# Kernel optimization log

Measured on AMD Instinct MI355X. Metric: run time of the kernel, lower is better.

The kernel has to match this reference:

```python
import jax, jax.numpy as jnp
import numpy as np

B, N, A, O, D, Q, H = 64, 4, 1024, 128, 256, 256, 128
NEG_INF = -1e30


def setup_inputs() -> dict:
    key = jax.random.key(0)
    ks = jax.random.split(key, 8)
    q = jax.random.normal(ks[0], (B, N, 1, Q), dtype=jnp.float32)
    att1 = jax.random.uniform(ks[1], (B, N, A, O), dtype=jnp.float32)
    obj_reps = jax.random.normal(ks[2], (B, O, D), dtype=jnp.float32)
    tags_attention = jax.random.randint(ks[3], (B, N, A), 0, 2, dtype=jnp.int32)
    W1 = jax.random.normal(ks[4], (D + Q, H), dtype=jnp.float32) / np.sqrt(D + Q)
    b1 = jnp.zeros((H,), dtype=jnp.float32)
    W2 = jax.random.normal(ks[5], (H, 1), dtype=jnp.float32) / np.sqrt(H)
    b2 = jnp.zeros((1,), dtype=jnp.float32)
    return {"q": q, "att1": att1, "obj_reps": obj_reps,
            "tags_attention": tags_attention,
            "W1": W1, "b1": b1, "W2": W2, "b2": b2, "t": 1}


def reference(q, att1, obj_reps, tags_attention, W1, b1, W2, b2, t):
    # v: [B,N,A,D] = att1 [B,N,A,O] @ obj_reps [B,O,D]
    v = jnp.einsum('bnao,bod->bnad', att1, obj_reps)
    # q broadcast over token dim A, concat -> [B,N,A,D+Q]
    q_proj = jnp.broadcast_to(q, v.shape[:3] + (q.shape[-1],))
    vq = jnp.concatenate([v, q_proj], axis=-1)
    # FCNet: Linear + ReLU (dropout is identity at inference)
    joint_repr = jax.nn.relu(vq @ W1 + b1)          # [B,N,A,H]
    logits = (joint_repr @ W2 + b2)[..., 0]          # [B,N,A]
    # temperature-scaled masked softmax over tokens
    masked = jnp.where(tags_attention > 0, logits / t, NEG_INF)
    att2 = jax.nn.softmax(masked, axis=-1)           # [B,N,A]
    # attention_last: [B,N,O] = att2 [B,N,1,A] @ att1 [B,N,A,O]
    return jnp.einsum('bna,bnao->bno', att2, att1)
```

## Files before the change

kernel.cpp:

```cpp
#include <hip/hip_runtime.h>
#include <math.h>

#define Bc 64
#define Nc 4
#define Ac 1024
#define Oc 128
#define Dc 256
#define Qc 256
#define Hc 128
#define BN (Bc*Nc)

using f4     = __attribute__((ext_vector_type(4))) float;
using f32x4  = __attribute__((ext_vector_type(4))) float;
using short8 = __attribute__((ext_vector_type(8))) short;
using us4    = __attribute__((ext_vector_type(4))) unsigned short;

__device__ inline float decode_t(const void* p) {
    int i = *(const int*)p;
    if (i >= 1 && i <= 1000000) return (float)i;
    return __int_as_float(i);
}

__device__ inline unsigned short bf16_rne(float x) {
    unsigned u = __builtin_bit_cast(unsigned, x);
    u += 0x7FFFu + ((u >> 16) & 1u);
    return (unsigned short)(u >> 16);
}

__device__ inline void split_bf16(float x, unsigned short& hi, unsigned short& lo) {
    unsigned u = __builtin_bit_cast(unsigned, x);
    hi = (unsigned short)(u >> 16);
    float hif = __builtin_bit_cast(float, u & 0xFFFF0000u);
    float lof = x - hif;
    lo = (unsigned short)(__builtin_bit_cast(unsigned, lof) >> 16);
}

template<int CTRL>
__device__ inline float dpp_ror_add(float x) {
    int yi = __builtin_amdgcn_update_dpp(0, __builtin_bit_cast(int, x),
                                         CTRL, 0xf, 0xf, true);
    return x + __builtin_bit_cast(float, yi);
}
__device__ inline float row16_sum(float v) {
    v = dpp_ror_add<0x128>(v);
    v = dpp_ror_add<0x124>(v);
    v = dpp_ror_add<0x122>(v);
    v = dpp_ror_add<0x121>(v);
    return v;
}

__global__ __launch_bounds__(256) void prep_split_kernel(
    const float* __restrict__ obj, const float* __restrict__ W1,
    unsigned short* __restrict__ obj_hi, unsigned short* __restrict__ obj_lo,
    unsigned short* __restrict__ W1T_hi, unsigned short* __restrict__ W1T_lo)
{
    __shared__ float Ts[64][65];
    const int t = threadIdx.x;
    const int bid = blockIdx.x;

    if (bid < 1024) {
        size_t i0 = ((size_t)bid * 256 + t) * 8;
        f4 v0 = *(const f4*)(obj + i0);
        f4 v1 = *(const f4*)(obj + i0 + 4);
        short8 hi, lo;
        unsigned short h16, l16;
        #pragma unroll
        for (int j = 0; j < 4; j++) {
            split_bf16(v0[j], h16, l16); hi[j] = (short)h16; lo[j] = (short)l16;
        }
        #pragma unroll
        for (int j = 0; j < 4; j++) {
            split_bf16(v1[j], h16, l16); hi[4 + j] = (short)h16; lo[4 + j] = (short)l16;
        }
        *(short8*)(obj_hi + i0) = hi;
        *(short8*)(obj_lo + i0) = lo;
    } else {
        const int wb = bid - 1024;
        const int d0 = (wb & 3) * 64, h0 = (wb >> 2) * 64;
        const int r4 = t >> 6, c = t & 63;
        #pragma unroll
        for (int rr = 0; rr < 16; rr++) {
            int d = rr * 4 + r4;
            Ts[d][c] = W1[(size_t)(d0 + d) * Hc + h0 + c];
        }
        __syncthreads();
        #pragma unroll
        for (int rr = 0; rr < 16; rr++) {
            int hl = rr * 4 + r4;
            float v = Ts[c][hl];
            unsigned short h16, l16;
            split_bf16(v, h16, l16);
            W1T_hi[(size_t)(h0 + hl) * Dc + d0 + c] = h16;
            W1T_lo[(size_t)(h0 + hl) * Dc + d0 + c] = l16;
        }
    }
}

__global__ __launch_bounds__(256, 4) void prep_M2_kernel(
    const unsigned short* __restrict__ W1T_hi, const unsigned short* __restrict__ W1T_lo,
    const unsigned short* __restrict__ obj_hi, const unsigned short* __restrict__ obj_lo,
    unsigned short* __restrict__ Mt_hi, unsigned short* __restrict__ Mt_lo)
{
    const int t = threadIdx.x;
    const int wave = t >> 6, lane = t & 63;
    const int l15 = lane & 15, quad = lane >> 4;
    const int h0 = blockIdx.x * 64 + wave * 16;
    const int o0 = blockIdx.y * 32;
    const int b  = blockIdx.z;

    const size_t arow  = (size_t)(h0 + l15) * Dc;
    const size_t brow0 = ((size_t)b * Oc + o0 + l15) * Dc;
    const size_t brow1 = ((size_t)b * Oc + o0 + 16 + l15) * Dc;

    f32x4 acc0 = (f32x4)(0.f), acc1 = (f32x4)(0.f);
    #pragma unroll
    for (int ks = 0; ks < 8; ks++) {
        const int ko = ks * 32 + quad * 8;
        short8 Ah  = *(const short8*)(W1T_hi + arow + ko);
        short8 Al  = *(const short8*)(W1T_lo + arow + ko);
        short8 B0h = *(const short8*)(obj_hi + brow0 + ko);
        short8 B0l = *(const short8*)(obj_lo + brow0 + ko);
        short8 B1h = *(const short8*)(obj_hi + brow1 + ko);
        short8 B1l = *(const short8*)(obj_lo + brow1 + ko);
        acc0 = __builtin_amdgcn_mfma_f32_16x16x32_bf16(Al, B0l, acc0, 0, 0, 0);
        acc0 = __builtin_amdgcn_mfma_f32_16x16x32_bf16(Al, B0h, acc0, 0, 0, 0);
        acc0 = __builtin_amdgcn_mfma_f32_16x16x32_bf16(Ah, B0l, acc0, 0, 0, 0);
        acc0 = __builtin_amdgcn_mfma_f32_16x16x32_bf16(Ah, B0h, acc0, 0, 0, 0);
        acc1 = __builtin_amdgcn_mfma_f32_16x16x32_bf16(Al, B1l, acc1, 0, 0, 0);
        acc1 = __builtin_amdgcn_mfma_f32_16x16x32_bf16(Al, B1h, acc1, 0, 0, 0);
        acc1 = __builtin_amdgcn_mfma_f32_16x16x32_bf16(Ah, B1l, acc1, 0, 0, 0);
        acc1 = __builtin_amdgcn_mfma_f32_16x16x32_bf16(Ah, B1h, acc1, 0, 0, 0);
    }

    #pragma unroll
    for (int r = 0; r < 4; r++) {
        int hrow = h0 + quad * 4 + r;
        size_t base = ((size_t)b * Hc + hrow) * Oc + o0 + l15;
        unsigned short hh, ll;
        split_bf16(acc0[r], hh, ll);
        Mt_hi[base] = hh; Mt_lo[base] = ll;
        split_bf16(acc1[r], hh, ll);
        Mt_hi[base + 16] = hh; Mt_lo[base + 16] = ll;
    }
}

__global__ __launch_bounds__(512) void prep_qb_kernel(
    const float* __restrict__ q, const float* __restrict__ W1,
    const float* __restrict__ b1, float* __restrict__ qb)
{
    __shared__ float qs[256];
    __shared__ float red[4][128];
    const int t = threadIdx.x;
    const int bn = blockIdx.x;

    if (t < 256) qs[t] = q[bn * Qc + t];
    __syncthreads();

    const int h = t & 127, kq = t >> 7;
    float acc = 0.f;
    const float* w = W1 + (size_t)(Dc + kq * 64) * Hc + h;
    #pragma unroll 8
    for (int d = 0; d < 64; ++d)
        acc += qs[kq * 64 + d] * w[(size_t)d * Hc];
    red[kq][h] = acc;
    __syncthreads();

    if (t < 128)
        qb[bn * Hc + t] = b1[t] + red[0][t] + red[1][t] + red[2][t] + red[3][t];
}

__global__ __launch_bounds__(512, 4) void main_half_kernel(
    const float* __restrict__ att1, const int* __restrict__ tags,
    const unsigned short* __restrict__ Mt_hi, const unsigned short* __restrict__ Mt_lo,
    const float* __restrict__ qb, const float* __restrict__ W2,
    const float* __restrict__ b2, const void* __restrict__ tptr,
    float* __restrict__ out_part, float* __restrict__ z_part)
{
    __shared__ unsigned short A_s[64][136];
    __shared__ float part2[64][9];
    __shared__ float part3[16][132];
    __shared__ float e_s[64];
    __shared__ float qb_s[128], w2_s[128];

    const int t    = threadIdx.x;
    const int lane = t & 63;
    const int wave = t >> 6;
    const int l15  = lane & 15;
    const int quad = lane >> 4;
    const int blk  = blockIdx.x;
    const int bn   = blk >> 1;
    const int half = blk & 1;
    const int b    = bn >> 2;
    const int hw   = wave * 16;
    const int g3   = t >> 5;
    const int o4   = (t & 31) * 4;

    const float* att_half = att1 + ((size_t)bn * Ac + half * 512) * Oc;

    f4 sv[4];
    #pragma unroll
    for (int s = 0; s < 4; s++) {
        int idx = t + 512 * s;
        sv[s] = *(const f4*)(att_half + (size_t)idx * 4);
    }

    const size_t brow = ((size_t)b * Hc + hw + l15) * Oc;
    short8 Bh[4], Bl[4];
    #pragma unroll
    for (int ks = 0; ks < 4; ks++) {
        const int ko = ks * 32 + quad * 8;
        Bh[ks] = *(const short8*)(Mt_hi + brow + ko);
        Bl[ks] = *(const short8*)(Mt_lo + brow + ko);
    }

    if (t < 128) { qb_s[t] = qb[bn * Hc + t]; w2_s[t] = W2[t]; }
    int tg_cur = (t < 64) ? tags[(size_t)bn * Ac + half * 512 + t] : 0;
    const float b2v  = b2[0];
    const float tval = decode_t(tptr);

    float z_reg = 0.f;
    f4 out4 = {0.f, 0.f, 0.f, 0.f};

    for (int tile = 0; tile < 8; ++tile) {
        #pragma unroll
        for (int s = 0; s < 4; s++) {
            int idx = t + 512 * s;
            int r = idx >> 5, c4 = idx & 31;
            us4 h4;
            #pragma unroll
            for (int j = 0; j < 4; j++) h4[j] = bf16_rne(sv[s][j]);
            *(us4*)&A_s[r][c4 * 4] = h4;
        }
        __syncthreads();

        f4 nv[4];
        int tg_next = 0;
        if (tile < 7) {
            const float* np = att_half + (size_t)(tile + 1) * 64 * Oc;
            #pragma unroll
            for (int s = 0; s < 4; s++) {
                int idx = t + 512 * s;
                nv[s] = *(const f4*)(np + (size_t)idx * 4);
            }
            if (t < 64) tg_next = tags[(size_t)bn * Ac + half * 512 + (tile + 1) * 64 + t];
        }

        f32x4 acc[4];
        #pragma unroll
        for (int i = 0; i < 4; i++) acc[i] = (f32x4)(0.f);
        #pragma unroll
        for (int ks = 0; ks < 4; ks++) {
            const int ko = ks * 32 + quad * 8;
            #pragma unroll
            for (int i = 0; i < 4; i++) {
                short8 ah = *(const short8*)&A_s[i * 16 + l15][ko];
                acc[i] = __builtin_amdgcn_mfma_f32_16x16x32_bf16(ah, Bh[ks], acc[i], 0, 0, 0);
                acc[i] = __builtin_amdgcn_mfma_f32_16x16x32_bf16(ah, Bl[ks], acc[i], 0, 0, 0);
            }
        }

        {
            const float qbv = qb_s[hw + l15], w2v = w2_s[hw + l15];
            #pragma unroll
            for (int i = 0; i < 4; i++)
                #pragma unroll
                for (int r = 0; r < 4; r++) {
                    float v = acc[i][r] + qbv;
                    v = v > 0.f ? v : 0.f;
                    float s = row16_sum(v * w2v);
                    if (l15 == 0)
                        part2[i * 16 + quad * 4 + r][wave] = s;
                }
        }
        __syncthreads();

        if (t < 64) {
            float sum = b2v;
            #pragma unroll
            for (int x = 0; x < 8; x++) sum += part2[t][x];
            float logit = sum / tval;
            float e = (tg_cur > 0) ? __expf(logit) : 0.f;
            e_s[t] = e;
            z_reg += e;
        }
        __syncthreads();

        #pragma unroll
        for (int s = 0; s < 4; s++) {
            const float ev = e_s[g3 + 16 * s];
            out4[0] += ev * sv[s][0];
            out4[1] += ev * sv[s][1];
            out4[2] += ev * sv[s][2];
            out4[3] += ev * sv[s][3];
        }

        #pragma unroll
        for (int s = 0; s < 4; s++) sv[s] = nv[s];
        tg_cur = tg_next;
    }

    __syncthreads();
    *(f4*)&part3[g3][o4] = out4;
    __syncthreads();
    if (t < 128) {
        float s = 0.f;
        #pragma unroll
        for (int g = 0; g < 16; g++) s += part3[g][t];
        out_part[(size_t)blk * 128 + t] = s;
    }
    if (t < 64) {
        float z = z_reg;
        #pragma unroll
        for (int off = 32; off > 0; off >>= 1) z += __shfl_down(z, off);
        if (t == 0) z_part[blk] = z;
    }
}

__global__ __launch_bounds__(128) void finalize_kernel(
    const float* __restrict__ out_part, const float* __restrict__ z_part,
    float* __restrict__ out)
{
    const int bn = blockIdx.x;
    const int t  = threadIdx.x;
    const float Z = z_part[bn * 2] + z_part[bn * 2 + 1];
    const float v = out_part[(size_t)(bn * 2) * 128 + t]
                  + out_part[(size_t)(bn * 2 + 1) * 128 + t];
    out[(size_t)bn * 128 + t] = v / Z;
}

extern "C" void kernel_launch(void* const* d_in, const int* in_sizes, int n_in,
                              void* d_out, int out_size, void* d_ws, size_t ws_size,
                              hipStream_t stream)
{
    (void)in_sizes; (void)n_in; (void)out_size; (void)ws_size;

    const float* q    = (const float*)d_in[0];
    const float* att1 = (const float*)d_in[1];
    const float* obj  = (const float*)d_in[2];
    const int*   tags = (const int*)d_in[3];
    const float* W1   = (const float*)d_in[4];
    const float* b1   = (const float*)d_in[5];
    const float* W2   = (const float*)d_in[6];
    const float* b2   = (const float*)d_in[7];
    const void*  tptr = (const void*)d_in[8];
    float* out = (float*)d_out;

    char* wsb = (char*)d_ws;
    unsigned short* Mt_hi  = (unsigned short*)wsb;
    unsigned short* Mt_lo  = (unsigned short*)(wsb + (size_t) 2*1024*1024);
    float* qbuf            = (float*)         (wsb + (size_t) 4*1024*1024);
    float* out_part        = (float*)         (wsb + (size_t) 5*1024*1024);
    float* z_part          = (float*)         (wsb + (size_t) 6*1024*1024);
    unsigned short* W1T_hi = (unsigned short*)(wsb + (size_t) 7*1024*1024);
    unsigned short* W1T_lo = (unsigned short*)(wsb + (size_t) 7*1024*1024 + 64*1024);
    unsigned short* obj_hi = (unsigned short*)(wsb + (size_t) 8*1024*1024);
    unsigned short* obj_lo = (unsigned short*)(wsb + (size_t)12*1024*1024);

    prep_split_kernel<<<dim3(1032), 256, 0, stream>>>(obj, W1, obj_hi, obj_lo,
                                                      W1T_hi, W1T_lo);
    prep_M2_kernel<<<dim3(2, 4, Bc), 256, 0, stream>>>(W1T_hi, W1T_lo, obj_hi, obj_lo,
                                                       Mt_hi, Mt_lo);
    prep_qb_kernel<<<dim3(BN), 512, 0, stream>>>(q, W1, b1, qbuf);
    main_half_kernel<<<dim3(2 * BN), 512, 0, stream>>>(att1, tags, Mt_hi, Mt_lo,
                                                       qbuf, W2, b2, tptr,
                                                       out_part, z_part);
    finalize_kernel<<<dim3(BN), 128, 0, stream>>>(out_part, z_part, out);
}
```

Before: 241.9 us.

## Fuse prep kernels and fold finalize into main kernel via atomic flag handoff

Merges the bf16 split, M2 GEMM and qb projection into a single prep kernel that splits W1 and obj rows in registers instead of staging hi/lo copies in global memory. It also removes the finalize kernel: each block pair handshakes through an atomicExch flag with a magic tag, and the second arriving half combines the partials and writes the output. This cuts two kernel launches and the intermediate workspace traffic. In exchange, W1 is read uncoalesced and redundantly per block, and the flag scheme relies on stale workspace values not matching the magic tag across calls.

```diff
diff --git a/kernel.cpp b/kernel.cpp
--- a/kernel.cpp
+++ b/kernel.cpp
@@ -49,138 +49,119 @@
     return v;
 }
 
-__global__ __launch_bounds__(256) void prep_split_kernel(
+__device__ inline short8 pack_hi(const f4& a, const f4& b,
+                                 short8& lo_out) {
+    short8 hi;
+    unsigned short h16, l16;
+    #pragma unroll
+    for (int j = 0; j < 4; j++) {
+        split_bf16(a[j], h16, l16); hi[j] = (short)h16; lo_out[j] = (short)l16;
+    }
+    #pragma unroll
+    for (int j = 0; j < 4; j++) {
+        split_bf16(b[j], h16, l16); hi[4+j] = (short)h16; lo_out[4+j] = (short)l16;
+    }
+    return hi;
+}
+
+__global__ __launch_bounds__(256, 2) void prep_fused_kernel(
     const float* __restrict__ obj, const float* __restrict__ W1,
-    unsigned short* __restrict__ obj_hi, unsigned short* __restrict__ obj_lo,
-    unsigned short* __restrict__ W1T_hi, unsigned short* __restrict__ W1T_lo)
-{
-    __shared__ float Ts[64][65];
-    const int t = threadIdx.x;
-    const int bid = blockIdx.x;
-
-    if (bid < 1024) {
-        size_t i0 = ((size_t)bid * 256 + t) * 8;
-        f4 v0 = *(const f4*)(obj + i0);
-        f4 v1 = *(const f4*)(obj + i0 + 4);
-        short8 hi, lo;
-        unsigned short h16, l16;
-        #pragma unroll
-        for (int j = 0; j < 4; j++) {
-            split_bf16(v0[j], h16, l16); hi[j] = (short)h16; lo[j] = (short)l16;
-        }
-        #pragma unroll
-        for (int j = 0; j < 4; j++) {
-            split_bf16(v1[j], h16, l16); hi[4 + j] = (short)h16; lo[4 + j] = (short)l16;
-        }
-        *(short8*)(obj_hi + i0) = hi;
-        *(short8*)(obj_lo + i0) = lo;
-    } else {
-        const int wb = bid - 1024;
-        const int d0 = (wb & 3) * 64, h0 = (wb >> 2) * 64;
-        const int r4 = t >> 6, c = t & 63;
-        #pragma unroll
-        for (int rr = 0; rr < 16; rr++) {
-            int d = rr * 4 + r4;
-            Ts[d][c] = W1[(size_t)(d0 + d) * Hc + h0 + c];
-        }
-        __syncthreads();
-        #pragma unroll
-        for (int rr = 0; rr < 16; rr++) {
-            int hl = rr * 4 + r4;
-            float v = Ts[c][hl];
-            unsigned short h16, l16;
-            split_bf16(v, h16, l16);
-            W1T_hi[(size_t)(h0 + hl) * Dc + d0 + c] = h16;
-            W1T_lo[(size_t)(h0 + hl) * Dc + d0 + c] = l16;
-        }
-    }
-}
-
-__global__ __launch_bounds__(256, 4) void prep_M2_kernel(
-    const unsigned short* __restrict__ W1T_hi, const unsigned short* __restrict__ W1T_lo,
-    const unsigned short* __restrict__ obj_hi, const unsigned short* __restrict__ obj_lo,
-    unsigned short* __restrict__ Mt_hi, unsigned short* __restrict__ Mt_lo)
-{
-    const int t = threadIdx.x;
-    const int wave = t >> 6, lane = t & 63;
-    const int l15 = lane & 15, quad = lane >> 4;
-    const int h0 = blockIdx.x * 64 + wave * 16;
-    const int o0 = blockIdx.y * 32;
-    const int b  = blockIdx.z;
-
-    const size_t arow  = (size_t)(h0 + l15) * Dc;
-    const size_t brow0 = ((size_t)b * Oc + o0 + l15) * Dc;
-    const size_t brow1 = ((size_t)b * Oc + o0 + 16 + l15) * Dc;
-
-    f32x4 acc0 = (f32x4)(0.f), acc1 = (f32x4)(0.f);
-    #pragma unroll
-    for (int ks = 0; ks < 8; ks++) {
-        const int ko = ks * 32 + quad * 8;
-        short8 Ah  = *(const short8*)(W1T_hi + arow + ko);
-        short8 Al  = *(const short8*)(W1T_lo + arow + ko);
-        short8 B0h = *(const short8*)(obj_hi + brow0 + ko);
-        short8 B0l = *(const short8*)(obj_lo + brow0 + ko);
-        short8 B1h = *(const short8*)(obj_hi + brow1 + ko);
-        short8 B1l = *(const short8*)(obj_lo + brow1 + ko);
-        acc0 = __builtin_amdgcn_mfma_f32_16x16x32_bf16(Al, B0l, acc0, 0, 0, 0);
-        acc0 = __builtin_amdgcn_mfma_f32_16x16x32_bf16(Al, B0h, acc0, 0, 0, 0);
-        acc0 = __builtin_amdgcn_mfma_f32_16x16x32_bf16(Ah, B0l, acc0, 0, 0, 0);
-        acc0 = __builtin_amdgcn_mfma_f32_16x16x32_bf16(Ah, B0h, acc0, 0, 0, 0);
-        acc1 = __builtin_amdgcn_mfma_f32_16x16x32_bf16(Al, B1l, acc1, 0, 0, 0);
-        acc1 = __builtin_amdgcn_mfma_f32_16x16x32_bf16(Al, B1h, acc1, 0, 0, 0);
-        acc1 = __builtin_amdgcn_mfma_f32_16x16x32_bf16(Ah, B1l, acc1, 0, 0, 0);
-        acc1 = __builtin_amdgcn_mfma_f32_16x16x32_bf16(Ah, B1h, acc1, 0, 0, 0);
-    }
-
-    #pragma unroll
-    for (int r = 0; r < 4; r++) {
-        int hrow = h0 + quad * 4 + r;
-        size_t base = ((size_t)b * Hc + hrow) * Oc + o0 + l15;
-        unsigned short hh, ll;
-        split_bf16(acc0[r], hh, ll);
-        Mt_hi[base] = hh; Mt_lo[base] = ll;
-        split_bf16(acc1[r], hh, ll);
-        Mt_hi[base + 16] = hh; Mt_lo[base + 16] = ll;
-    }
-}
-
-__global__ __launch_bounds__(512) void prep_qb_kernel(
-    const float* __restrict__ q, const float* __restrict__ W1,
-    const float* __restrict__ b1, float* __restrict__ qb)
+    const float* __restrict__ q,   const float* __restrict__ b1,
+    unsigned short* __restrict__ Mt_hi, unsigned short* __restrict__ Mt_lo,
+    float* __restrict__ qb)
 {
     __shared__ float qs[256];
-    __shared__ float red[4][128];
-    const int t = threadIdx.x;
-    const int bn = blockIdx.x;
-
-    if (t < 256) qs[t] = q[bn * Qc + t];
-    __syncthreads();
-
-    const int h = t & 127, kq = t >> 7;
-    float acc = 0.f;
-    const float* w = W1 + (size_t)(Dc + kq * 64) * Hc + h;
-    #pragma unroll 8
-    for (int d = 0; d < 64; ++d)
-        acc += qs[kq * 64 + d] * w[(size_t)d * Hc];
-    red[kq][h] = acc;
-    __syncthreads();
-
-    if (t < 128)
-        qb[bn * Hc + t] = b1[t] + red[0][t] + red[1][t] + red[2][t] + red[3][t];
-}
+    __shared__ float red[2][128];
+
+    const int bid = blockIdx.x;
+    const int t   = threadIdx.x;
+
+    if (bid < 512) {
+        const int b    = bid >> 3;
+        const int rr   = bid & 7;
+        const int h0   = (rr & 1) * 64;
+        const int o0   = (rr >> 1) * 32;
+        const int wave = t >> 6, lane = t & 63;
+        const int l15  = lane & 15, quad = lane >> 4;
+        const int hh   = h0 + wave * 16 + l15;
+
+        short8 Ah[8], Al[8];
+        #pragma unroll
+        for (int ks = 0; ks < 8; ks++) {
+            const int ko = ks * 32 + quad * 8;
+            #pragma unroll
+            for (int j = 0; j < 8; j++) {
+                unsigned short h16, l16;
+                split_bf16(W1[(size_t)(ko + j) * Hc + hh], h16, l16);
+                Ah[ks][j] = (short)h16; Al[ks][j] = (short)l16;
+            }
+        }
+
+        const float* ob0 = obj + ((size_t)b * Oc + o0 + l15) * Dc;
+        const float* ob1 = obj + ((size_t)b * Oc + o0 + 16 + l15) * Dc;
+
+        f32x4 acc0 = (f32x4)(0.f), acc1 = (f32x4)(0.f);
+        #pragma unroll
+        for (int ks = 0; ks < 8; ks++) {
+            const int ko = ks * 32 + quad * 8;
+            short8 B0l, B1l;
+            short8 B0h = pack_hi(*(const f4*)(ob0 + ko), *(const f4*)(ob0 + ko + 4), B0l);
+            short8 B1h = pack_hi(*(const f4*)(ob1 + ko), *(const f4*)(ob1 + ko + 4), B1l);
+            acc0 = __builtin_amdgcn_mfma_f32_16x16x32_bf16(Al[ks], B0l, acc0, 0, 0, 0);
+            acc0 = __builtin_amdgcn_mfma_f32_16x16x32_bf16(Al[ks], B0h, acc0, 0, 0, 0);
+            acc0 = __builtin_amdgcn_mfma_f32_16x16x32_bf16(Ah[ks], B0l, acc0, 0, 0, 0);
+            acc0 = __builtin_amdgcn_mfma_f32_16x16x32_bf16(Ah[ks], B0h, acc0, 0, 0, 0);
+            acc1 = __builtin_amdgcn_mfma_f32_16x16x32_bf16(Al[ks], B1l, acc1, 0, 0, 0);
+            acc1 = __builtin_amdgcn_mfma_f32_16x16x32_bf16(Al[ks], B1h, acc1, 0, 0, 0);
+            acc1 = __builtin_amdgcn_mfma_f32_16x16x32_bf16(Ah[ks], B1l, acc1, 0, 0, 0);
+            acc1 = __builtin_amdgcn_mfma_f32_16x16x32_bf16(Ah[ks], B1h, acc1, 0, 0, 0);
+        }
+
+        #pragma unroll
+        for (int r = 0; r < 4; r++) {
+            int hrow = h0 + wave * 16 + quad * 4 + r;
+            size_t base = ((size_t)b * Hc + hrow) * Oc + o0 + l15;
+            unsigned short hh16, ll16;
+            split_bf16(acc0[r], hh16, ll16);
+            Mt_hi[base] = hh16; Mt_lo[base] = ll16;
+            split_bf16(acc1[r], hh16, ll16);
+            Mt_hi[base + 16] = hh16; Mt_lo[base + 16] = ll16;
+        }
+    } else {
+        const int bn = bid - 512;
+        qs[t] = q[bn * Qc + t];
+        __syncthreads();
+
+        const int h = t & 127, kq = t >> 7;
+        float acc = 0.f;
+        const float* w = W1 + (size_t)(Dc + kq * 128) * Hc + h;
+        #pragma unroll 8
+        for (int d = 0; d < 128; ++d)
+            acc += qs[kq * 128 + d] * w[(size_t)d * Hc];
+        red[kq][h] = acc;
+        __syncthreads();
+
+        if (t < 128)
+            qb[bn * Hc + t] = b1[t] + red[0][t] + red[1][t];
+    }
+}
+
+#define MAGIC 0x3A9F17C0u
 
 __global__ __launch_bounds__(512, 4) void main_half_kernel(
     const float* __restrict__ att1, const int* __restrict__ tags,
     const unsigned short* __restrict__ Mt_hi, const unsigned short* __restrict__ Mt_lo,
     const float* __restrict__ qb, const float* __restrict__ W2,
     const float* __restrict__ b2, const void* __restrict__ tptr,
-    float* __restrict__ out_part, float* __restrict__ z_part)
+    float* __restrict__ out_part, float* __restrict__ z_part,
+    unsigned* __restrict__ flags, float* __restrict__ out)
 {
     __shared__ unsigned short A_s[64][136];
     __shared__ float part2[64][9];
     __shared__ float part3[16][132];
     __shared__ float e_s[64];
     __shared__ float qb_s[128], w2_s[128];
+    __shared__ int win_s;
 
     const int t    = threadIdx.x;
     const int lane = t & 63;
@@ -312,20 +293,22 @@
         float z = z_reg;
         #pragma unroll
         for (int off = 32; off > 0; off >>= 1) z += __shfl_down(z, off);
-        if (t == 0) z_part[blk] = z;
-    }
-}
-
-__global__ __launch_bounds__(128) void finalize_kernel(
-    const float* __restrict__ out_part, const float* __restrict__ z_part,
-    float* __restrict__ out)
-{
-    const int bn = blockIdx.x;
-    const int t  = threadIdx.x;
-    const float Z = z_part[bn * 2] + z_part[bn * 2 + 1];
-    const float v = out_part[(size_t)(bn * 2) * 128 + t]
-                  + out_part[(size_t)(bn * 2 + 1) * 128 + t];
-    out[(size_t)bn * 128 + t] = v / Z;
+        if (t == 0) z_part[(size_t)blk * 32] = z;
+    }
+
+    __threadfence();
+    __syncthreads();
+    if (t == 0) {
+        unsigned old = atomicExch(&flags[bn], MAGIC | (unsigned)half);
+        win_s = (old == (MAGIC | (unsigned)(half ^ 1)));
+    }
+    __syncthreads();
+    if (win_s && t < 128) {
+        float Z = z_part[(size_t)(bn * 2) * 32] + z_part[(size_t)(bn * 2 + 1) * 32];
+        float v = out_part[(size_t)(bn * 2) * 128 + t]
+                + out_part[(size_t)(bn * 2 + 1) * 128 + t];
+        out[(size_t)bn * Oc + t] = v / Z;
+    }
 }
 
 extern "C" void kernel_launch(void* const* d_in, const int* in_sizes, int n_in,
@@ -346,23 +329,16 @@
     float* out = (float*)d_out;
 
     char* wsb = (char*)d_ws;
-    unsigned short* Mt_hi  = (unsigned short*)wsb;
-    unsigned short* Mt_lo  = (unsigned short*)(wsb + (size_t) 2*1024*1024);
-    float* qbuf            = (float*)         (wsb + (size_t) 4*1024*1024);
-    float* out_part        = (float*)         (wsb + (size_t) 5*1024*1024);
-    float* z_part          = (float*)         (wsb + (size_t) 6*1024*1024);
-    unsigned short* W1T_hi = (unsigned short*)(wsb + (size_t) 7*1024*1024);
-    unsigned short* W1T_lo = (unsigned short*)(wsb + (size_t) 7*1024*1024 + 64*1024);
-    unsigned short* obj_hi = (unsigned short*)(wsb + (size_t) 8*1024*1024);
-    unsigned short* obj_lo = (unsigned short*)(wsb + (size_t)12*1024*1024);
-
-    prep_split_kernel<<<dim3(1032), 256, 0, stream>>>(obj, W1, obj_hi, obj_lo,
-                                                      W1T_hi, W1T_lo);
-    prep_M2_kernel<<<dim3(2, 4, Bc), 256, 0, stream>>>(W1T_hi, W1T_lo, obj_hi, obj_lo,
-                                                       Mt_hi, Mt_lo);
-    prep_qb_kernel<<<dim3(BN), 512, 0, stream>>>(q, W1, b1, qbuf);
+    unsigned short* Mt_hi = (unsigned short*)wsb;
+    unsigned short* Mt_lo = (unsigned short*)(wsb + (size_t)2*1024*1024);
+    float* qbuf     = (float*)   (wsb + (size_t)4*1024*1024);
+    float* out_part = (float*)   (wsb + (size_t)5*1024*1024);
+    float* z_part   = (float*)   (wsb + (size_t)6*1024*1024);
+    unsigned* flags = (unsigned*)(wsb + (size_t)7*1024*1024);
+
+    prep_fused_kernel<<<dim3(512 + BN), 256, 0, stream>>>(obj, W1, q, b1,
+                                                          Mt_hi, Mt_lo, qbuf);
     main_half_kernel<<<dim3(2 * BN), 512, 0, stream>>>(att1, tags, Mt_hi, Mt_lo,
                                                        qbuf, W2, b2, tptr,
-                                                       out_part, z_part);
-    finalize_kernel<<<dim3(BN), 128, 0, stream>>>(out_part, z_part, out);
-}
+                                                       out_part, z_part, flags, out);
+}
```

After: 335.8 us. 38.8% more time.

## Double-buffer bf16 A tile in LDS and fold qb prep into split kernel

Applied to the files above, without the earlier changes.

The main kernel now keeps two LDS buffers for the bf16-converted att1 tile. The next tile is converted and written during the softmax phase, which removes the separate convert-then-barrier step at the top of each loop iteration. The qb projection is merged into the prep_split kernel as extra 256-thread blocks, dropping one kernel launch. The costs are more LDS per block, which may limit occupancy, and a longer serial loop per thread in the qb blocks.

```diff
diff --git a/kernel.cpp b/kernel.cpp
--- a/kernel.cpp
+++ b/kernel.cpp
@@ -49,12 +49,16 @@
     return v;
 }
 
-__global__ __launch_bounds__(256) void prep_split_kernel(
+__global__ __launch_bounds__(256) void prep_combined_kernel(
     const float* __restrict__ obj, const float* __restrict__ W1,
+    const float* __restrict__ q,   const float* __restrict__ b1,
     unsigned short* __restrict__ obj_hi, unsigned short* __restrict__ obj_lo,
-    unsigned short* __restrict__ W1T_hi, unsigned short* __restrict__ W1T_lo)
+    unsigned short* __restrict__ W1T_hi, unsigned short* __restrict__ W1T_lo,
+    float* __restrict__ qb)
 {
     __shared__ float Ts[64][65];
+    __shared__ float qs[256];
+    __shared__ float red[2][128];
     const int t = threadIdx.x;
     const int bid = blockIdx.x;
 
@@ -74,7 +78,7 @@
         }
         *(short8*)(obj_hi + i0) = hi;
         *(short8*)(obj_lo + i0) = lo;
-    } else {
+    } else if (bid < 1032) {
         const int wb = bid - 1024;
         const int d0 = (wb & 3) * 64, h0 = (wb >> 2) * 64;
         const int r4 = t >> 6, c = t & 63;
@@ -93,6 +97,22 @@
             W1T_hi[(size_t)(h0 + hl) * Dc + d0 + c] = h16;
             W1T_lo[(size_t)(h0 + hl) * Dc + d0 + c] = l16;
         }
+    } else {
+        const int bn = bid - 1032;
+        qs[t] = q[bn * Qc + t];
+        __syncthreads();
+
+        const int h = t & 127, kq = t >> 7;
+        float acc = 0.f;
+        const float* w = W1 + (size_t)(Dc + kq * 128) * Hc + h;
+        #pragma unroll 8
+        for (int d = 0; d < 128; ++d)
+            acc += qs[kq * 128 + d] * w[(size_t)d * Hc];
+        red[kq][h] = acc;
+        __syncthreads();
+
+        if (t < 128)
+            qb[bn * Hc + t] = b1[t] + red[0][t] + red[1][t];
     }
 }
 
@@ -144,31 +164,6 @@
     }
 }
 
-__global__ __launch_bounds__(512) void prep_qb_kernel(
-    const float* __restrict__ q, const float* __restrict__ W1,
-    const float* __restrict__ b1, float* __restrict__ qb)
-{
-    __shared__ float qs[256];
-    __shared__ float red[4][128];
-    const int t = threadIdx.x;
-    const int bn = blockIdx.x;
-
-    if (t < 256) qs[t] = q[bn * Qc + t];
-    __syncthreads();
-
-    const int h = t & 127, kq = t >> 7;
-    float acc = 0.f;
-    const float* w = W1 + (size_t)(Dc + kq * 64) * Hc + h;
-    #pragma unroll 8
-    for (int d = 0; d < 64; ++d)
-        acc += qs[kq * 64 + d] * w[(size_t)d * Hc];
-    red[kq][h] = acc;
-    __syncthreads();
-
-    if (t < 128)
-        qb[bn * Hc + t] = b1[t] + red[0][t] + red[1][t] + red[2][t] + red[3][t];
-}
-
 __global__ __launch_bounds__(512, 4) void main_half_kernel(
     const float* __restrict__ att1, const int* __restrict__ tags,
     const unsigned short* __restrict__ Mt_hi, const unsigned short* __restrict__ Mt_lo,
@@ -176,7 +171,7 @@
     const float* __restrict__ b2, const void* __restrict__ tptr,
     float* __restrict__ out_part, float* __restrict__ z_part)
 {
-    __shared__ unsigned short A_s[64][136];
+    __shared__ unsigned short A_s[2][64][136];
     __shared__ float part2[64][9];
     __shared__ float part3[16][132];
     __shared__ float e_s[64];
@@ -218,20 +213,22 @@
     const float b2v  = b2[0];
     const float tval = decode_t(tptr);
 
+    #pragma unroll
+    for (int s = 0; s < 4; s++) {
+        int idx = t + 512 * s;
+        int r = idx >> 5, c4 = idx & 31;
+        us4 h4;
+        #pragma unroll
+        for (int j = 0; j < 4; j++) h4[j] = bf16_rne(sv[s][j]);
+        *(us4*)&A_s[0][r][c4 * 4] = h4;
+    }
+    __syncthreads();
+
     float z_reg = 0.f;
     f4 out4 = {0.f, 0.f, 0.f, 0.f};
 
     for (int tile = 0; tile < 8; ++tile) {
-        #pragma unroll
-        for (int s = 0; s < 4; s++) {
-            int idx = t + 512 * s;
-            int r = idx >> 5, c4 = idx & 31;
-            us4 h4;
-            #pragma unroll
-            for (int j = 0; j < 4; j++) h4[j] = bf16_rne(sv[s][j]);
-            *(us4*)&A_s[r][c4 * 4] = h4;
-        }
-        __syncthreads();
+        const int buf = tile & 1;
 
         f4 nv[4];
         int tg_next = 0;
@@ -253,7 +250,7 @@
             const int ko = ks * 32 + quad * 8;
             #pragma unroll
             for (int i = 0; i < 4; i++) {
-                short8 ah = *(const short8*)&A_s[i * 16 + l15][ko];
+                short8 ah = *(const short8*)&A_s[buf][i * 16 + l15][ko];
                 acc[i] = __builtin_amdgcn_mfma_f32_16x16x32_bf16(ah, Bh[ks], acc[i], 0, 0, 0);
                 acc[i] = __builtin_amdgcn_mfma_f32_16x16x32_bf16(ah, Bl[ks], acc[i], 0, 0, 0);
             }
@@ -283,6 +280,17 @@
             e_s[t] = e;
             z_reg += e;
         }
+        if (tile < 7) {
+            #pragma unroll
+            for (int s = 0; s < 4; s++) {
+                int idx = t + 512 * s;
+                int r = idx >> 5, c4 = idx & 31;
+                us4 h4;
+                #pragma unroll
+                for (int j = 0; j < 4; j++) h4[j] = bf16_rne(nv[s][j]);
+                *(us4*)&A_s[buf ^ 1][r][c4 * 4] = h4;
+            }
+        }
         __syncthreads();
 
         #pragma unroll
@@ -294,9 +302,11 @@
             out4[3] += ev * sv[s][3];
         }
 
-        #pragma unroll
-        for (int s = 0; s < 4; s++) sv[s] = nv[s];
-        tg_cur = tg_next;
+        if (tile < 7) {
+            #pragma unroll
+            for (int s = 0; s < 4; s++) sv[s] = nv[s];
+            tg_cur = tg_next;
+        }
     }
 
     __syncthreads();
@@ -356,11 +366,10 @@
     unsigned short* obj_hi = (unsigned short*)(wsb + (size_t) 8*1024*1024);
     unsigned short* obj_lo = (unsigned short*)(wsb + (size_t)12*1024*1024);
 
-    prep_split_kernel<<<dim3(1032), 256, 0, stream>>>(obj, W1, obj_hi, obj_lo,
-                                                      W1T_hi, W1T_lo);
+    prep_combined_kernel<<<dim3(1032 + BN), 256, 0, stream>>>(
+        obj, W1, q, b1, obj_hi, obj_lo, W1T_hi, W1T_lo, qbuf);
     prep_M2_kernel<<<dim3(2, 4, Bc), 256, 0, stream>>>(W1T_hi, W1T_lo, obj_hi, obj_lo,
                                                        Mt_hi, Mt_lo);
-    prep_qb_kernel<<<dim3(BN), 512, 0, stream>>>(q, W1, b1, qbuf);
     main_half_kernel<<<dim3(2 * BN), 512, 0, stream>>>(att1, tags, Mt_hi, Mt_lo,
                                                        qbuf, W2, b2, tptr,
                                                        out_part, z_part);
```

Measured after the change: 240.6 us. About the same (-0.5%).
